# Kernel optimization log

Hardware: AMD Instinct MI355X
Metric: run time of the kernel (lower is better)

The kernel has to match this reference:

```python
import jax, jax.numpy as jnp
import numpy as np


def setup_inputs() -> dict:
    key = jax.random.key(0)
    k1, k2 = jax.random.split(key)
    B, S, D = 16, 2048, 128
    x1 = jax.random.normal(k1, (B, S, D), dtype=jnp.float32)
    x2 = jax.random.normal(k2, (B, S, D), dtype=jnp.float32)
    return {"x1": x1, "x2": x2}


def reference(x1, x2):
    # Mutual cross attention (eval mode, dropout is identity).
    d = x1.shape[-1]
    scale = 1.0 / jnp.sqrt(jnp.asarray(d, dtype=x1.dtype))
    # scores[b,i,j] = <x1[b,i], x2[b,j]> / sqrt(d). The second score matrix in the
    # original (key @ query^T) is exactly the transpose, so compute once.
    scores = jnp.einsum("bid,bjd->bij", x1, x2) * scale  # [B,S,S]
    out_A = jnp.einsum("bij,bjd->bid", jax.nn.softmax(scores, axis=-1), x2)
    # softmax over rows of scores^T == softmax over axis -2 of scores, then transpose
    out_B = jnp.einsum("bij,bid->bjd", jax.nn.softmax(scores, axis=-2), x1)
    return out_A + out_B
```

## Files before the change

### kernel.cpp

```cpp
#include <hip/hip_runtime.h>

typedef _Float16 f16;
typedef f16 f16x8 __attribute__((ext_vector_type(8)));
typedef f16 f16x4 __attribute__((ext_vector_type(4)));
typedef float f32x4 __attribute__((ext_vector_type(4)));

#define MFMA_F16(a, b, c) __builtin_amdgcn_mfma_f32_16x16x32_f16((a), (b), (c), 0, 0, 0)

namespace {
constexpr int SN = 2048;
constexpr int DN = 128;
constexpr int KVB = 64;
constexpr int NW = 4;
constexpr int QW = 32;
constexpr int QB = NW * QW;
constexpr float SCALE_L2E = 0.1275213897f;
}

__device__ __forceinline__ int kidx(int kv, int d)  { return kv * DN  + (d  ^ ((kv & 7) << 3)); }
__device__ __forceinline__ int vidx(int d, int kv)  { return d  * KVB + (kv ^ (((d ^ (d >> 3)) & 7) << 3)); }
__device__ __forceinline__ int pidx(int q, int kv)  { return q  * KVB + (kv ^ ((q  & 7) << 3)); }

__global__ __launch_bounds__(256, 2)
void mca_kernel(const float* __restrict__ x1, const float* __restrict__ x2,
                float* __restrict__ out)
{
    __shared__ __align__(16) f16 sK[KVB * DN];
    __shared__ __align__(16) f16 sV[DN * KVB];
    __shared__ __align__(16) f16 sP[NW * QW * KVB];

    const int gid  = blockIdx.x;
    const int work = (gid & 7) * 64 + (gid >> 3);
    const int pass = work >> 8;
    const int b    = (work >> 4) & 15;
    const int q0   = (work & 15) * QB;

    const int t  = threadIdx.x;
    const int w  = t >> 6;
    const int l  = t & 63;
    const int lg = l >> 4;
    const int ll = l & 15;

    const int rg = t >> 4;
    const int cg = t & 15;

    f16* sPw = sP + w * (QW * KVB);

    const float* xq  = pass ? x2 : x1;
    const float* xkv = pass ? x1 : x2;
    const float* qb  = xq  + ((size_t)b * SN + q0 + w * QW) * DN;
    const float* kb  = xkv + (size_t)b * SN * DN;

    f16x8 qf[2][4];
    #pragma unroll
    for (int nq = 0; nq < 2; ++nq)
        #pragma unroll
        for (int kk = 0; kk < 4; ++kk) {
            const float* p = qb + (nq * 16 + ll) * DN + kk * 32 + lg * 8;
            float4 a0 = *(const float4*)p;
            float4 a1 = *(const float4*)(p + 4);
            f16x8 q;
            q[0] = (f16)(a0.x * SCALE_L2E); q[1] = (f16)(a0.y * SCALE_L2E);
            q[2] = (f16)(a0.z * SCALE_L2E); q[3] = (f16)(a0.w * SCALE_L2E);
            q[4] = (f16)(a1.x * SCALE_L2E); q[5] = (f16)(a1.y * SCALE_L2E);
            q[6] = (f16)(a1.z * SCALE_L2E); q[7] = (f16)(a1.w * SCALE_L2E);
            qf[nq][kk] = q;
        }

    f32x4 oAcc[2][8];
    #pragma unroll
    for (int a = 0; a < 2; ++a)
        #pragma unroll
        for (int n = 0; n < 8; ++n) oAcc[a][n] = (f32x4){0.f, 0.f, 0.f, 0.f};
    float mrun[2] = {-1e30f, -1e30f};
    float lrun[2] = {0.f, 0.f};

    for (int kv0 = 0; kv0 < SN; kv0 += KVB) {
        __syncthreads();
        {
            const float* src = kb + (size_t)kv0 * DN;
            float hv[4][8];
            #pragma unroll
            for (int rr = 0; rr < 4; ++rr) {
                const float* p = src + (4 * rg + rr) * DN + 8 * cg;
                float4 a0 = *(const float4*)p;
                float4 a1 = *(const float4*)(p + 4);
                hv[rr][0] = a0.x; hv[rr][1] = a0.y; hv[rr][2] = a0.z; hv[rr][3] = a0.w;
                hv[rr][4] = a1.x; hv[rr][5] = a1.y; hv[rr][6] = a1.z; hv[rr][7] = a1.w;
            }
            #pragma unroll
            for (int rr = 0; rr < 4; ++rr) {
                f16x8 kp;
                #pragma unroll
                for (int j = 0; j < 8; ++j) kp[j] = (f16)hv[rr][j];
                *(f16x8*)&sK[kidx(4 * rg + rr, 8 * cg)] = kp;
            }
            #pragma unroll
            for (int i = 0; i < 8; ++i) {
                f16x4 vp;
                #pragma unroll
                for (int rr = 0; rr < 4; ++rr) vp[rr] = (f16)hv[rr][i];
                *(f16x4*)&sV[vidx(8 * cg + i, 4 * rg)] = vp;
            }
        }
        __syncthreads();

        f32x4 sacc[4][2];
        #pragma unroll
        for (int mt = 0; mt < 4; ++mt)
            #pragma unroll
            for (int nq = 0; nq < 2; ++nq) sacc[mt][nq] = (f32x4){0.f, 0.f, 0.f, 0.f};
        #pragma unroll
        for (int kk = 0; kk < 4; ++kk) {
            #pragma unroll
            for (int mt = 0; mt < 4; ++mt) {
                f16x8 ka = *(const f16x8*)&sK[kidx(mt * 16 + ll, kk * 32 + lg * 8)];
                sacc[mt][0] = MFMA_F16(ka, qf[0][kk], sacc[mt][0]);
                sacc[mt][1] = MFMA_F16(ka, qf[1][kk], sacc[mt][1]);
            }
        }

        #pragma unroll
        for (int nq = 0; nq < 2; ++nq) {
            const int q = nq * 16 + ll;
            float tm = sacc[0][nq][0];
            #pragma unroll
            for (int mt = 0; mt < 4; ++mt)
                #pragma unroll
                for (int r = 0; r < 4; ++r) tm = fmaxf(tm, sacc[mt][nq][r]);
            tm = fmaxf(tm, __shfl_xor(tm, 16));
            tm = fmaxf(tm, __shfl_xor(tm, 32));
            float mnew = fmaxf(mrun[nq], tm);
            float corr = exp2f(mrun[nq] - mnew);
            float ps = 0.f;
            #pragma unroll
            for (int mt = 0; mt < 4; ++mt) {
                f16x4 pk;
                #pragma unroll
                for (int r = 0; r < 4; ++r) {
                    float pv = exp2f(sacc[mt][nq][r] - mnew);
                    ps += pv;
                    pk[r] = (f16)pv;
                }
                *(f16x4*)&sPw[pidx(q, mt * 16 + 4 * lg)] = pk;
            }
            ps += __shfl_xor(ps, 16);
            ps += __shfl_xor(ps, 32);
            lrun[nq] = lrun[nq] * corr + ps;
            mrun[nq] = mnew;
            #pragma unroll
            for (int r = 0; r < 4; ++r) {
                float c2 = __shfl(corr, 4 * lg + r);
                #pragma unroll
                for (int nd = 0; nd < 8; ++nd) oAcc[nq][nd][r] *= c2;
            }
        }

        f16x8 pa[2][2];
        #pragma unroll
        for (int mq = 0; mq < 2; ++mq)
            #pragma unroll
            for (int kc = 0; kc < 2; ++kc)
                pa[mq][kc] = *(const f16x8*)&sPw[pidx(mq * 16 + ll, kc * 32 + lg * 8)];
        #pragma unroll
        for (int nd = 0; nd < 8; ++nd) {
            #pragma unroll
            for (int kc = 0; kc < 2; ++kc) {
                f16x8 vb = *(const f16x8*)&sV[vidx(nd * 16 + ll, kc * 32 + lg * 8)];
                oAcc[0][nd] = MFMA_F16(pa[0][kc], vb, oAcc[0][nd]);
                oAcc[1][nd] = MFMA_F16(pa[1][kc], vb, oAcc[1][nd]);
            }
        }
    }

    float* ob = out + ((size_t)b * SN + q0 + w * QW) * DN;
    #pragma unroll
    for (int mq = 0; mq < 2; ++mq)
        #pragma unroll
        for (int r = 0; r < 4; ++r) {
            float li = __shfl(lrun[mq], 4 * lg + r);
            float inv = 1.0f / li;
            const int row = mq * 16 + 4 * lg + r;
            #pragma unroll
            for (int nd = 0; nd < 8; ++nd)
                atomicAdd(&ob[row * DN + nd * 16 + ll], oAcc[mq][nd][r] * inv);
        }
}

extern "C" void kernel_launch(void* const* d_in, const int* in_sizes, int n_in,
                              void* d_out, int out_size, void* d_ws, size_t ws_size,
                              hipStream_t stream) {
    const float* x1 = (const float*)d_in[0];
    const float* x2 = (const float*)d_in[1];
    float* out = (float*)d_out;
    const int B = in_sizes[0] / (SN * DN);
    hipMemsetAsync(d_out, 0, (size_t)out_size * sizeof(float), stream);
    dim3 grid(2 * B * (SN / QB));
    dim3 block(256);
    hipLaunchKernelGGL(mca_kernel, grid, block, 0, stream, x1, x2, out);
}
```

Measured before the change: 147.4 us.

## Double-buffer K/V shared tiles and prefetch next tile into registers

Doubles the K and V shared-memory buffers and issues the global loads for the next KV tile before computing on the current one. The loaded values are converted and written to the alternate buffer after softmax, and each iteration now ends with one barrier instead of two. The aim is to hide global load latency behind the MFMA work. In exchange, LDS use grows from about 48KB to 80KB per block, which may cut the two-blocks-per-CU occupancy, and the 32 prefetched floats per thread raise register pressure.

```diff
diff --git a/kernel.cpp b/kernel.cpp
--- a/kernel.cpp
+++ b/kernel.cpp
@@ -11,6 +11,7 @@
 constexpr int SN = 2048;
 constexpr int DN = 128;
 constexpr int KVB = 64;
+constexpr int NT = SN / KVB;
 constexpr int NW = 4;
 constexpr int QW = 32;
 constexpr int QB = NW * QW;
@@ -25,8 +26,8 @@
 void mca_kernel(const float* __restrict__ x1, const float* __restrict__ x2,
                 float* __restrict__ out)
 {
-    __shared__ __align__(16) f16 sK[KVB * DN];
-    __shared__ __align__(16) f16 sV[DN * KVB];
+    __shared__ __align__(16) f16 sK[2][KVB * DN];
+    __shared__ __align__(16) f16 sV[2][DN * KVB];
     __shared__ __align__(16) f16 sP[NW * QW * KVB];
 
     const int gid  = blockIdx.x;
@@ -67,6 +68,36 @@
             qf[nq][kk] = q;
         }
 
+    float hv[4][8];
+
+    auto LOAD = [&](int tile) {
+        const float* src = kb + (size_t)tile * KVB * DN;
+        #pragma unroll
+        for (int rr = 0; rr < 4; ++rr) {
+            const float* p = src + (4 * rg + rr) * DN + 8 * cg;
+            float4 a0 = *(const float4*)p;
+            float4 a1 = *(const float4*)(p + 4);
+            hv[rr][0] = a0.x; hv[rr][1] = a0.y; hv[rr][2] = a0.z; hv[rr][3] = a0.w;
+            hv[rr][4] = a1.x; hv[rr][5] = a1.y; hv[rr][6] = a1.z; hv[rr][7] = a1.w;
+        }
+    };
+    auto WRITE = [&](f16* Kb, f16* Vb) {
+        #pragma unroll
+        for (int rr = 0; rr < 4; ++rr) {
+            f16x8 kp;
+            #pragma unroll
+            for (int j = 0; j < 8; ++j) kp[j] = (f16)hv[rr][j];
+            *(f16x8*)&Kb[kidx(4 * rg + rr, 8 * cg)] = kp;
+        }
+        #pragma unroll
+        for (int i = 0; i < 8; ++i) {
+            f16x4 vp;
+            #pragma unroll
+            for (int rr = 0; rr < 4; ++rr) vp[rr] = (f16)hv[rr][i];
+            *(f16x4*)&Vb[vidx(8 * cg + i, 4 * rg)] = vp;
+        }
+    };
+
     f32x4 oAcc[2][8];
     #pragma unroll
     for (int a = 0; a < 2; ++a)
@@ -75,35 +106,16 @@
     float mrun[2] = {-1e30f, -1e30f};
     float lrun[2] = {0.f, 0.f};
 
-    for (int kv0 = 0; kv0 < SN; kv0 += KVB) {
-        __syncthreads();
-        {
-            const float* src = kb + (size_t)kv0 * DN;
-            float hv[4][8];
-            #pragma unroll
-            for (int rr = 0; rr < 4; ++rr) {
-                const float* p = src + (4 * rg + rr) * DN + 8 * cg;
-                float4 a0 = *(const float4*)p;
-                float4 a1 = *(const float4*)(p + 4);
-                hv[rr][0] = a0.x; hv[rr][1] = a0.y; hv[rr][2] = a0.z; hv[rr][3] = a0.w;
-                hv[rr][4] = a1.x; hv[rr][5] = a1.y; hv[rr][6] = a1.z; hv[rr][7] = a1.w;
-            }
-            #pragma unroll
-            for (int rr = 0; rr < 4; ++rr) {
-                f16x8 kp;
-                #pragma unroll
-                for (int j = 0; j < 8; ++j) kp[j] = (f16)hv[rr][j];
-                *(f16x8*)&sK[kidx(4 * rg + rr, 8 * cg)] = kp;
-            }
-            #pragma unroll
-            for (int i = 0; i < 8; ++i) {
-                f16x4 vp;
-                #pragma unroll
-                for (int rr = 0; rr < 4; ++rr) vp[rr] = (f16)hv[rr][i];
-                *(f16x4*)&sV[vidx(8 * cg + i, 4 * rg)] = vp;
-            }
-        }
-        __syncthreads();
+    LOAD(0);
+    WRITE(sK[0], sV[0]);
+    __syncthreads();
+
+    for (int tile = 0; tile < NT; ++tile) {
+        const int cur = tile & 1;
+        const f16* Kc = sK[cur];
+        const f16* Vc = sV[cur];
+
+        if (tile + 1 < NT) LOAD(tile + 1);
 
         f32x4 sacc[4][2];
         #pragma unroll
@@ -114,7 +126,7 @@
         for (int kk = 0; kk < 4; ++kk) {
             #pragma unroll
             for (int mt = 0; mt < 4; ++mt) {
-                f16x8 ka = *(const f16x8*)&sK[kidx(mt * 16 + ll, kk * 32 + lg * 8)];
+                f16x8 ka = *(const f16x8*)&Kc[kidx(mt * 16 + ll, kk * 32 + lg * 8)];
                 sacc[mt][0] = MFMA_F16(ka, qf[0][kk], sacc[mt][0]);
                 sacc[mt][1] = MFMA_F16(ka, qf[1][kk], sacc[mt][1]);
             }
@@ -156,6 +168,8 @@
             }
         }
 
+        if (tile + 1 < NT) WRITE(sK[cur ^ 1], sV[cur ^ 1]);
+
         f16x8 pa[2][2];
         #pragma unroll
         for (int mq = 0; mq < 2; ++mq)
@@ -166,11 +180,13 @@
         for (int nd = 0; nd < 8; ++nd) {
             #pragma unroll
             for (int kc = 0; kc < 2; ++kc) {
-                f16x8 vb = *(const f16x8*)&sV[vidx(nd * 16 + ll, kc * 32 + lg * 8)];
+                f16x8 vb = *(const f16x8*)&Vc[vidx(nd * 16 + ll, kc * 32 + lg * 8)];
                 oAcc[0][nd] = MFMA_F16(pa[0][kc], vb, oAcc[0][nd]);
                 oAcc[1][nd] = MFMA_F16(pa[1][kc], vb, oAcc[1][nd]);
             }
         }
+
+        __syncthreads();
     }
 
     float* ob = out + ((size_t)b * SN + q0 + w * QW) * DN;
```

Result: no change. 147.0 us (-0.3%).
